# Performance work log

Measured on AMD Instinct MI355X. Metric: run time of the kernel, lower is better.

## Reference

```python
import jax, jax.numpy as jnp
import numpy as np

N_NODES = 50000


def gcn_conv(x, W, b, src, dst, n_nodes):
    """GCNConv (PyG defaults): h = D^{-1/2}(A+I)D^{-1/2} (x @ W) + b, edge weights = 1.
    Self loops handled analytically (self-loop norm = 1/deg_i) to avoid growing edge arrays."""
    h = x @ W  # [N, out]
    # degree including self loop, computed on destination (col) per PyG gcn_norm
    deg = jax.ops.segment_sum(jnp.ones(src.shape[0], h.dtype), dst, num_segments=n_nodes) + 1.0
    dinv = jax.lax.rsqrt(deg)  # deg >= 1 so no clamping needed
    norm = dinv[src] * dinv[dst]  # [E]
    agg = jax.ops.segment_sum(h[src] * norm[:, None], dst, num_segments=n_nodes)
    agg = agg + h * (dinv * dinv)[:, None]  # self-loop contribution
    return agg + b


def setup_inputs() -> dict:
    key = jax.random.key(0)
    ks = jax.random.split(key, 6)
    n, e, d_in, d_hid = N_NODES, 800000, 128, 16
    x = jax.random.normal(ks[0], (n, d_in), dtype=jnp.float32)
    edge_index = jax.random.randint(ks[1], (2, e), 0, n, dtype=jnp.int64)
    W1 = jax.random.normal(ks[2], (d_in, d_hid), dtype=jnp.float32) * (1.0 / np.sqrt(d_in))
    b1 = jnp.zeros((d_hid,), jnp.float32)
    W2 = jax.random.normal(ks[3], (d_hid, d_in), dtype=jnp.float32) * (1.0 / np.sqrt(d_hid))
    b2 = jnp.zeros((d_in,), jnp.float32)
    return {"x": x, "edge_index": edge_index, "W1": W1, "b1": b1, "W2": W2, "b2": b2}


def reference(x, edge_index, W1, b1, W2, b2):
    src, dst = edge_index[0], edge_index[1]
    z = gcn_conv(x, W1, b1, src, dst, N_NODES)          # encoder: 128 -> 16
    recon = gcn_conv(z, W2, b2, src, dst, N_NODES)      # decoder: 16 -> 128
    return recon
```

## Files before the change

kernel.cpp:

```cpp
#include <hip/hip_runtime.h>


#define N_NODES 50000
#define N_EDGES 800000
#define D_IN    128
#define D_H     16
#define K_BUCK  256
#define NPB2    196
#define BSHIFT  12
#define BCAP    (1 << BSHIFT)
#define GC_PAD  16
#define G_BLKS  196
#define SC_BLKS 316
#define SC_CH   2536
#define SC_I4   634
#define K4_NPB  128

#define PACKH(pk, d) { \
    int c0 = d.x / NPB2, c1 = d.y / NPB2, c2 = d.z / NPB2, c3 = d.w / NPB2; \
    pk.x = (c0 << 8) | (d.x - c0 * NPB2); pk.y = (c1 << 8) | (d.y - c1 * NPB2); \
    pk.z = (c2 << 8) | (d.z - c2 * NPB2); pk.w = (c3 << 8) | (d.w - c3 * NPB2); \
    atomicAdd(&hist[c0], 1); atomicAdd(&hist[c1], 1); \
    atomicAdd(&hist[c2], 1); atomicAdd(&hist[c3], 1); }

#define SCAT(pk, sv) { \
    int c0 = pk.x >> 8, c1 = pk.y >> 8, c2 = pk.z >> 8, c3 = pk.w >> 8; \
    int q0 = atomicAdd(&cur[c0], 1); int q1 = atomicAdd(&cur[c1], 1); \
    int q2 = atomicAdd(&cur[c2], 1); int q3 = atomicAdd(&cur[c3], 1); \
    if (q0 < ((c0 + 1) << BSHIFT)) arr[q0] = (sv.x << 8) | (pk.x & 255); \
    if (q1 < ((c1 + 1) << BSHIFT)) arr[q1] = (sv.y << 8) | (pk.y & 255); \
    if (q2 < ((c2 + 1) << BSHIFT)) arr[q2] = (sv.z << 8) | (pk.z & 255); \
    if (q3 < ((c3 + 1) << BSHIFT)) arr[q3] = (sv.w << 8) | (pk.w & 255); }

__global__ __launch_bounds__(256) void k1_fused(
        const int* __restrict__ src, const int* __restrict__ dst,
        const float* __restrict__ x, const float* __restrict__ W1,
        int* __restrict__ gcur, float* __restrict__ h1, int* __restrict__ arr) {
    __shared__ __align__(16) float w1s[D_IN * D_H];
    __shared__ int hist[K_BUCK];
    __shared__ int cur[K_BUCK];
    int bid = blockIdx.x;
    int tid = threadIdx.x;

    if (bid < G_BLKS) {
        for (int i = tid; i < D_IN * D_H; i += 256) w1s[i] = W1[i];
        __syncthreads();
        int row = bid * 256 + tid;
        if (row >= N_NODES) return;
        const float4* xr = (const float4*)(x + row * D_IN);
        const float4* w4 = (const float4*)w1s;
        float4 a0 = {0, 0, 0, 0}, a1 = a0, a2 = a0, a3 = a0;
        for (int k4 = 0; k4 < D_IN / 4; ++k4) {
            float4 xv = xr[k4];
            #pragma unroll
            for (int j = 0; j < 4; ++j) {
                float xk = (j == 0) ? xv.x : (j == 1) ? xv.y : (j == 2) ? xv.z : xv.w;
                const float4* wr = w4 + (k4 * 4 + j) * 4;
                float4 w0 = wr[0], w1v = wr[1], w2v = wr[2], w3v = wr[3];
                a0.x += xk * w0.x;  a0.y += xk * w0.y;  a0.z += xk * w0.z;  a0.w += xk * w0.w;
                a1.x += xk * w1v.x; a1.y += xk * w1v.y; a1.z += xk * w1v.z; a1.w += xk * w1v.w;
                a2.x += xk * w2v.x; a2.y += xk * w2v.y; a2.z += xk * w2v.z; a2.w += xk * w2v.w;
                a3.x += xk * w3v.x; a3.y += xk * w3v.y; a3.z += xk * w3v.z; a3.w += xk * w3v.w;
            }
        }
        float4* hr = (float4*)(h1 + row * D_H);
        hr[0] = a0; hr[1] = a1; hr[2] = a2; hr[3] = a3;
    } else {
        int base_e = (bid - G_BLKS) * SC_CH;
        int ni4 = min((N_EDGES - base_e) >> 2, SC_I4);
        for (int b = tid; b < K_BUCK; b += 256) hist[b] = 0;
        __syncthreads();
        const int4* d4p = (const int4*)(dst + base_e);
        const int4* s4p = (const int4*)(src + base_e);
        int4 pk0, pk1, pk2;
        bool a0 = tid < ni4, a1 = tid + 256 < ni4, a2 = tid + 512 < ni4;
        if (a0) { int4 d = d4p[tid];       PACKH(pk0, d); }
        if (a1) { int4 d = d4p[tid + 256]; PACKH(pk1, d); }
        if (a2) { int4 d = d4p[tid + 512]; PACKH(pk2, d); }
        __syncthreads();
        if (tid < K_BUCK)
            cur[tid] = (tid << BSHIFT) + atomicAdd(&gcur[tid * GC_PAD], hist[tid]);
        __syncthreads();
        if (a0) { int4 sv = s4p[tid];       SCAT(pk0, sv); }
        if (a1) { int4 sv = s4p[tid + 256]; SCAT(pk1, sv); }
        if (a2) { int4 sv = s4p[tid + 512]; SCAT(pk2, sv); }
    }
}

__global__ __launch_bounds__(512) void k2_build_csr(
        const int* __restrict__ arr, const int* __restrict__ gcur,
        float* __restrict__ h1, float* __restrict__ dinv,
        int* __restrict__ csr, int2* __restrict__ meta) {
    __shared__ int sarr[BCAP];
    __shared__ int cnt[NPB2];
    __shared__ int pref[NPB2];
    __shared__ int cur[NPB2];
    __shared__ float sdi[NPB2];
    int k = blockIdx.x, tid = threadIdx.x;
    for (int i = tid; i < NPB2; i += 512) cnt[i] = 0;
    __syncthreads();
    int count = min(gcur[k * GC_PAD], BCAP);
    int base = k << BSHIFT;
    for (int i = tid; i < count; i += 512) {
        int v = arr[base + i];
        sarr[i] = v;
        atomicAdd(&cnt[v & 255], 1);
    }
    __syncthreads();
    if (tid == 0) {
        int run = 0;
        for (int l = 0; l < NPB2; ++l) { pref[l] = run; run += cnt[l]; }
    }
    __syncthreads();
    int n0 = k * NPB2;
    int ncnt = min(NPB2, N_NODES - n0);
    for (int l = tid; l < ncnt; l += 512) {
        cur[l] = pref[l];
        meta[n0 + l] = make_int2(base + pref[l], cnt[l]);
        float di = rsqrtf((float)cnt[l] + 1.0f);
        sdi[l] = di;
        dinv[n0 + l] = di;
    }
    __syncthreads();
    for (int g = tid; g < ncnt * 4; g += 512) {
        int l = g >> 2;
        float di = sdi[l];
        float4* p = (float4*)(h1 + (n0 + l) * D_H);
        float4 v = p[g & 3];
        v.x *= di; v.y *= di; v.z *= di; v.w *= di;
        p[g & 3] = v;
    }
    for (int i = tid; i < count; i += 512) {
        int p = sarr[i];
        int l = p & 255;
        int pos = atomicAdd(&cur[l], 1);
        csr[base + pos] = p >> 8;
    }
}

__global__ __launch_bounds__(256) void k3_agg_enc(
        const float4* __restrict__ h1s4, const int* __restrict__ csr,
        const int2* __restrict__ meta, const float* __restrict__ dinv,
        const float* __restrict__ b1, float4* __restrict__ zs4) {
    int tid = threadIdx.x;
    int q = tid & 3;
    int n = blockIdx.x * 64 + (tid >> 2);
    if (n >= N_NODES) return;
    int qb = tid & 60;
    int2 m = meta[n];
    int e = m.x, end = m.x + m.y;
    float4 acc = {0.0f, 0.0f, 0.0f, 0.0f};
    for (; e < end; e += 4) {
        int myidx = 0;
        if (e + q < end) myidx = csr[e + q];
        #pragma unroll
        for (int j = 0; j < 4; ++j) {
            int idx = __shfl(myidx, qb + j, 64);
            if (e + j < end) {
                float4 v = h1s4[idx * 4 + q];
                acc.x += v.x; acc.y += v.y; acc.z += v.z; acc.w += v.w;
            }
        }
    }
    float di = dinv[n];
    float4 hv = h1s4[n * 4 + q];
    float4 bv = ((const float4*)b1)[q];
    float4 z;
    z.x = di * (di * (acc.x + hv.x) + bv.x);
    z.y = di * (di * (acc.y + hv.y) + bv.y);
    z.z = di * (di * (acc.z + hv.z) + bv.z);
    z.w = di * (di * (acc.w + hv.w) + bv.w);
    zs4[n * 4 + q] = z;
}

__global__ __launch_bounds__(512) void k4_agg_dec_out(
        const float4* __restrict__ zs4, const int* __restrict__ csr,
        const int2* __restrict__ meta, const float* __restrict__ dinv,
        const float* __restrict__ W2, const float* __restrict__ b2,
        float* __restrict__ out) {
    __shared__ float agL[K4_NPB * 17];
    __shared__ __align__(16) float w2s[D_H * D_IN];
    int tid = threadIdx.x;
    for (int i = tid; i < D_H * D_IN; i += 512) w2s[i] = W2[i];
    int q = tid & 3;
    int nloc = tid >> 2;
    int n0 = blockIdx.x * K4_NPB;
    int n = n0 + nloc;
    int qb = tid & 60;
    if (n < N_NODES) {
        int2 m = meta[n];
        int e = m.x, end = m.x + m.y;
        float4 acc = {0.0f, 0.0f, 0.0f, 0.0f};
        for (; e < end; e += 4) {
            int myidx = 0;
            if (e + q < end) myidx = csr[e + q];
            #pragma unroll
            for (int j = 0; j < 4; ++j) {
                int idx = __shfl(myidx, qb + j, 64);
                if (e + j < end) {
                    float4 v = zs4[idx * 4 + q];
                    acc.x += v.x; acc.y += v.y; acc.z += v.z; acc.w += v.w;
                }
            }
        }
        float di = dinv[n];
        float4 zv = zs4[n * 4 + q];
        agL[nloc * 17 + q * 4 + 0] = di * (acc.x + zv.x);
        agL[nloc * 17 + q * 4 + 1] = di * (acc.y + zv.y);
        agL[nloc * 17 + q * 4 + 2] = di * (acc.z + zv.z);
        agL[nloc * 17 + q * 4 + 3] = di * (acc.w + zv.w);
    }
    __syncthreads();
    int quarter = tid >> 7;
    int ne = tid & 127;
    if (n0 + ne < N_NODES) {
        const float* arow = &agL[ne * 17];
        float4 o[8];
        const float4* b2q = (const float4*)(b2 + quarter * 32);
        #pragma unroll
        for (int u = 0; u < 8; ++u) o[u] = b2q[u];
        #pragma unroll
        for (int c = 0; c < D_H; ++c) {
            float ac = arow[c];
            const float4* wr = (const float4*)(w2s + c * D_IN + quarter * 32);
            #pragma unroll
            for (int u = 0; u < 8; ++u) {
                float4 w = wr[u];
                o[u].x += ac * w.x; o[u].y += ac * w.y;
                o[u].z += ac * w.z; o[u].w += ac * w.w;
            }
        }
        float4* orow = (float4*)(out + (n0 + ne) * D_IN + quarter * 32);
        #pragma unroll
        for (int u = 0; u < 8; ++u) orow[u] = o[u];
    }
}

extern "C" void kernel_launch(void* const* d_in, const int* in_sizes, int n_in,
                              void* d_out, int out_size, void* d_ws, size_t ws_size,
                              hipStream_t stream) {
    const float* x  = (const float*)d_in[0];
    const int*   ei = (const int*)d_in[1];
    const float* W1 = (const float*)d_in[2];
    const float* b1 = (const float*)d_in[3];
    const float* W2 = (const float*)d_in[4];
    const float* b2 = (const float*)d_in[5];
    float* out = (float*)d_out;

    const int* src = ei;
    const int* dst = ei + N_EDGES;

    char* base = (char*)d_ws;
    int*    gcur = (int*)base;                 base += K_BUCK * GC_PAD * 4;
    float*  dinv = (float*)base;               base += N_NODES * 4;
    float*  h1   = (float*)base;               base += N_NODES * D_H * 4;
    float*  zs   = (float*)base;               base += N_NODES * D_H * 4;
    int2*   meta = (int2*)base;                base += N_NODES * 8;
    int*    arr  = (int*)base;                 base += K_BUCK * BCAP * 4;
    int*    csr  = (int*)base;                 base += K_BUCK * BCAP * 4;

    hipMemsetAsync(gcur, 0, K_BUCK * GC_PAD * sizeof(int), stream);

    k1_fused<<<G_BLKS + SC_BLKS, 256, 0, stream>>>(src, dst, x, W1, gcur, h1, arr);
    k2_build_csr<<<K_BUCK, 512, 0, stream>>>(arr, gcur, h1, dinv, csr, meta);
    k3_agg_enc<<<(N_NODES + 63) / 64, 256, 0, stream>>>((const float4*)h1, csr, meta, dinv, b1, (float4*)zs);
    k4_agg_dec_out<<<(N_NODES + K4_NPB - 1) / K4_NPB, 512, 0, stream>>>((const float4*)zs, csr, meta, dinv, W2, b2, out);
}
```

Before: 150.7 us.

## Use larger buckets and split CSR build into two half-blocks per bucket

```diff
diff --git a/kernel.cpp b/kernel.cpp
--- a/kernel.cpp
+++ b/kernel.cpp
@@ -5,34 +5,36 @@
 #define N_EDGES 800000
 #define D_IN    128
 #define D_H     16
-#define K_BUCK  256
-#define NPB2    196
-#define BSHIFT  12
+#define K_BUCK  128
+#define NPB2    391
+#define BSHIFT  13
 #define BCAP    (1 << BSHIFT)
 #define GC_PAD  16
-#define G_BLKS  196
-#define SC_BLKS 316
-#define SC_CH   2536
-#define SC_I4   634
+#define G_BLKS  98
+#define SC_BLKS 158
+#define SC_CH   5072
+#define SC_I4   1268
+#define NTHR    512
 #define K4_NPB  128
+#define HALF_N  196
 
 #define PACKH(pk, d) { \
     int c0 = d.x / NPB2, c1 = d.y / NPB2, c2 = d.z / NPB2, c3 = d.w / NPB2; \
-    pk.x = (c0 << 8) | (d.x - c0 * NPB2); pk.y = (c1 << 8) | (d.y - c1 * NPB2); \
-    pk.z = (c2 << 8) | (d.z - c2 * NPB2); pk.w = (c3 << 8) | (d.w - c3 * NPB2); \
+    pk.x = (c0 << 9) | (d.x - c0 * NPB2); pk.y = (c1 << 9) | (d.y - c1 * NPB2); \
+    pk.z = (c2 << 9) | (d.z - c2 * NPB2); pk.w = (c3 << 9) | (d.w - c3 * NPB2); \
     atomicAdd(&hist[c0], 1); atomicAdd(&hist[c1], 1); \
     atomicAdd(&hist[c2], 1); atomicAdd(&hist[c3], 1); }
 
 #define SCAT(pk, sv) { \
-    int c0 = pk.x >> 8, c1 = pk.y >> 8, c2 = pk.z >> 8, c3 = pk.w >> 8; \
+    int c0 = pk.x >> 9, c1 = pk.y >> 9, c2 = pk.z >> 9, c3 = pk.w >> 9; \
     int q0 = atomicAdd(&cur[c0], 1); int q1 = atomicAdd(&cur[c1], 1); \
     int q2 = atomicAdd(&cur[c2], 1); int q3 = atomicAdd(&cur[c3], 1); \
-    if (q0 < ((c0 + 1) << BSHIFT)) arr[q0] = (sv.x << 8) | (pk.x & 255); \
-    if (q1 < ((c1 + 1) << BSHIFT)) arr[q1] = (sv.y << 8) | (pk.y & 255); \
-    if (q2 < ((c2 + 1) << BSHIFT)) arr[q2] = (sv.z << 8) | (pk.z & 255); \
-    if (q3 < ((c3 + 1) << BSHIFT)) arr[q3] = (sv.w << 8) | (pk.w & 255); }
-
-__global__ __launch_bounds__(256) void k1_fused(
+    if (q0 < ((c0 + 1) << BSHIFT)) arr[q0] = (sv.x << 9) | (pk.x & 511); \
+    if (q1 < ((c1 + 1) << BSHIFT)) arr[q1] = (sv.y << 9) | (pk.y & 511); \
+    if (q2 < ((c2 + 1) << BSHIFT)) arr[q2] = (sv.z << 9) | (pk.z & 511); \
+    if (q3 < ((c3 + 1) << BSHIFT)) arr[q3] = (sv.w << 9) | (pk.w & 511); }
+
+__global__ __launch_bounds__(NTHR) void k1_fused(
         const int* __restrict__ src, const int* __restrict__ dst,
         const float* __restrict__ x, const float* __restrict__ W1,
         int* __restrict__ gcur, float* __restrict__ h1, int* __restrict__ arr) {
@@ -43,9 +45,9 @@
     int tid = threadIdx.x;
 
     if (bid < G_BLKS) {
-        for (int i = tid; i < D_IN * D_H; i += 256) w1s[i] = W1[i];
-        __syncthreads();
-        int row = bid * 256 + tid;
+        for (int i = tid; i < D_IN * D_H; i += NTHR) w1s[i] = W1[i];
+        __syncthreads();
+        int row = bid * NTHR + tid;
         if (row >= N_NODES) return;
         const float4* xr = (const float4*)(x + row * D_IN);
         const float4* w4 = (const float4*)w1s;
@@ -68,26 +70,26 @@
     } else {
         int base_e = (bid - G_BLKS) * SC_CH;
         int ni4 = min((N_EDGES - base_e) >> 2, SC_I4);
-        for (int b = tid; b < K_BUCK; b += 256) hist[b] = 0;
+        if (tid < K_BUCK) hist[tid] = 0;
         __syncthreads();
         const int4* d4p = (const int4*)(dst + base_e);
         const int4* s4p = (const int4*)(src + base_e);
         int4 pk0, pk1, pk2;
-        bool a0 = tid < ni4, a1 = tid + 256 < ni4, a2 = tid + 512 < ni4;
-        if (a0) { int4 d = d4p[tid];       PACKH(pk0, d); }
-        if (a1) { int4 d = d4p[tid + 256]; PACKH(pk1, d); }
-        if (a2) { int4 d = d4p[tid + 512]; PACKH(pk2, d); }
+        bool a0 = tid < ni4, a1 = tid + 512 < ni4, a2 = tid + 1024 < ni4;
+        if (a0) { int4 d = d4p[tid];        PACKH(pk0, d); }
+        if (a1) { int4 d = d4p[tid + 512];  PACKH(pk1, d); }
+        if (a2) { int4 d = d4p[tid + 1024]; PACKH(pk2, d); }
         __syncthreads();
         if (tid < K_BUCK)
             cur[tid] = (tid << BSHIFT) + atomicAdd(&gcur[tid * GC_PAD], hist[tid]);
         __syncthreads();
-        if (a0) { int4 sv = s4p[tid];       SCAT(pk0, sv); }
-        if (a1) { int4 sv = s4p[tid + 256]; SCAT(pk1, sv); }
-        if (a2) { int4 sv = s4p[tid + 512]; SCAT(pk2, sv); }
-    }
-}
-
-__global__ __launch_bounds__(512) void k2_build_csr(
+        if (a0) { int4 sv = s4p[tid];        SCAT(pk0, sv); }
+        if (a1) { int4 sv = s4p[tid + 512];  SCAT(pk1, sv); }
+        if (a2) { int4 sv = s4p[tid + 1024]; SCAT(pk2, sv); }
+    }
+}
+
+__global__ __launch_bounds__(NTHR) void k2_build_csr(
         const int* __restrict__ arr, const int* __restrict__ gcur,
         float* __restrict__ h1, float* __restrict__ dinv,
         int* __restrict__ csr, int2* __restrict__ meta) {
@@ -95,16 +97,18 @@
     __shared__ int cnt[NPB2];
     __shared__ int pref[NPB2];
     __shared__ int cur[NPB2];
-    __shared__ float sdi[NPB2];
-    int k = blockIdx.x, tid = threadIdx.x;
-    for (int i = tid; i < NPB2; i += 512) cnt[i] = 0;
+    __shared__ float sdi[HALF_N];
+    int k = blockIdx.x >> 1;
+    int half = blockIdx.x & 1;
+    int tid = threadIdx.x;
+    for (int i = tid; i < NPB2; i += NTHR) cnt[i] = 0;
     __syncthreads();
     int count = min(gcur[k * GC_PAD], BCAP);
     int base = k << BSHIFT;
-    for (int i = tid; i < count; i += 512) {
+    for (int i = tid; i < count; i += NTHR) {
         int v = arr[base + i];
         sarr[i] = v;
-        atomicAdd(&cnt[v & 255], 1);
+        atomicAdd(&cnt[v & 511], 1);
     }
     __syncthreads();
     if (tid == 0) {
@@ -112,29 +116,35 @@
         for (int l = 0; l < NPB2; ++l) { pref[l] = run; run += cnt[l]; }
     }
     __syncthreads();
-    int n0 = k * NPB2;
-    int ncnt = min(NPB2, N_NODES - n0);
-    for (int l = tid; l < ncnt; l += 512) {
+    int n0k = k * NPB2;
+    int l0 = half * HALF_N;
+    int hn = half ? min(NPB2 - HALF_N, max(0, N_NODES - n0k - HALF_N))
+                  : min(HALF_N, max(0, N_NODES - n0k));
+    for (int j = tid; j < hn; j += NTHR) {
+        int l = l0 + j;
         cur[l] = pref[l];
-        meta[n0 + l] = make_int2(base + pref[l], cnt[l]);
+        meta[n0k + l] = make_int2(base + pref[l], cnt[l]);
         float di = rsqrtf((float)cnt[l] + 1.0f);
-        sdi[l] = di;
-        dinv[n0 + l] = di;
-    }
-    __syncthreads();
-    for (int g = tid; g < ncnt * 4; g += 512) {
-        int l = g >> 2;
-        float di = sdi[l];
-        float4* p = (float4*)(h1 + (n0 + l) * D_H);
+        sdi[j] = di;
+        dinv[n0k + l] = di;
+    }
+    __syncthreads();
+    for (int g = tid; g < hn * 4; g += NTHR) {
+        int j = g >> 2;
+        float di = sdi[j];
+        float4* p = (float4*)(h1 + (n0k + l0 + j) * D_H);
         float4 v = p[g & 3];
         v.x *= di; v.y *= di; v.z *= di; v.w *= di;
         p[g & 3] = v;
     }
-    for (int i = tid; i < count; i += 512) {
+    int lend = l0 + hn;
+    for (int i = tid; i < count; i += NTHR) {
         int p = sarr[i];
-        int l = p & 255;
-        int pos = atomicAdd(&cur[l], 1);
-        csr[base + pos] = p >> 8;
+        int l = p & 511;
+        if (l >= l0 && l < lend) {
+            int pos = atomicAdd(&cur[l], 1);
+            csr[base + pos] = p >> 9;
+        }
     }
 }
 
@@ -261,8 +271,8 @@
 
     hipMemsetAsync(gcur, 0, K_BUCK * GC_PAD * sizeof(int), stream);
 
-    k1_fused<<<G_BLKS + SC_BLKS, 256, 0, stream>>>(src, dst, x, W1, gcur, h1, arr);
-    k2_build_csr<<<K_BUCK, 512, 0, stream>>>(arr, gcur, h1, dinv, csr, meta);
+    k1_fused<<<G_BLKS + SC_BLKS, NTHR, 0, stream>>>(src, dst, x, W1, gcur, h1, arr);
+    k2_build_csr<<<K_BUCK * 2, NTHR, 0, stream>>>(arr, gcur, h1, dinv, csr, meta);
     k3_agg_enc<<<(N_NODES + 63) / 64, 256, 0, stream>>>((const float4*)h1, csr, meta, dinv, b1, (float4*)zs);
     k4_agg_dec_out<<<(N_NODES + K4_NPB - 1) / K4_NPB, 512, 0, stream>>>((const float4*)zs, csr, meta, dinv, W2, b2, out);
 }
```

Result: slower. 158.6 us (+5.2%).
